# Optimization experiments

Hardware: AMD Instinct MI355X
Metric: run time of the kernel (lower is better)

The kernel has to match this reference:

```python
import jax, jax.numpy as jnp
import numpy as np

B, S, D, H = 4, 2048, 1024, 4
HD = D // H


def setup_inputs() -> dict:
    key = jax.random.key(0)
    ks = jax.random.split(key, 6)
    s = 0.02  # init scale for projection weights
    return {
        "hidden_states": jax.random.normal(ks[0], (B, S, D), jnp.float32),
        "Wq": jax.random.normal(ks[1], (D, D), jnp.float32) * s,
        "Wk": jax.random.normal(ks[2], (D, D), jnp.float32) * s,
        "Wv": jax.random.normal(ks[3], (D, D), jnp.float32) * s,
        "Wo": jax.random.normal(ks[4], (D, D), jnp.float32) * s,
        "bo": jnp.zeros((D,), jnp.float32),
        "betas": jax.random.normal(ks[5], (1, H, 1, 1), jnp.float32),
        "mem": jnp.zeros((H, HD, HD), jnp.float32),
        "z": jnp.zeros((H, HD, 1), jnp.float32),
    }


def reference(hidden_states, Wq, Wk, Wv, Wo, bo, betas, mem, z):
    b, s, d = hidden_states.shape
    h = betas.shape[1]
    hd = d // h

    def split(x):  # [b,s,d] -> [b,h,s,hd]
        return x.reshape(b, s, h, hd).transpose(0, 2, 1, 3)

    q = split(hidden_states @ Wq.T)
    k = split(hidden_states @ Wk.T)
    v = split(hidden_states @ Wv.T)

    # standard causal attention (note: no 1/sqrt(d) scaling, faithful to source)
    aw = jnp.einsum('bhqd,bhkd->bhqk', q, k)
    causal = jnp.tril(jnp.ones((s, s), bool))
    aw = jnp.where(causal, aw, jnp.finfo(aw.dtype).min)
    p = jax.nn.softmax(aw, axis=-1)
    attn = jnp.einsum('bhqk,bhkd->bhqd', p, v)

    # linear-attention memory read
    sq = jax.nn.elu(q) + 1.0
    sk = jax.nn.elu(k) + 1.0
    A_mem = jnp.einsum('bhsd,hde->bhse', sq, mem) / (
        jnp.einsum('bhsd,hdo->bhso', sq, z) + 1e-6)

    # sigmoid-gated blend
    g = jax.nn.sigmoid(betas)
    out = g * A_mem + (1.0 - g) * attn

    # memory / z state update (delta rule), averaged over batch
    delta = jnp.einsum('bhsd,hde->bhse', sk, mem) / (
        jnp.einsum('bhsd,hdo->bhso', sk, z) + 1e-6)
    mem_new = mem + jnp.einsum('bhsd,bhse->hde', sk, v - delta) / b
    z_new = z + jnp.mean(jnp.sum(sk, axis=2), axis=0)[:, :, None]

    # merge heads + output projection
    out = out.transpose(0, 2, 1, 3).reshape(b, s, d)
    out = out @ Wo.T + bo
    return (out, mem_new, z_new)
```

## Files before the change

kernel.cpp:

```cpp
#include <hip/hip_runtime.h>

#define Bsz 4
#define Ssz 2048
#define Dsz 1024
#define Hsz 4
#define HDsz 256
#define Msz 8192
#define LOG2E 1.4426950408889634f

typedef unsigned short u16;
typedef __attribute__((ext_vector_type(8))) short bf16x8;
typedef __attribute__((ext_vector_type(4))) float f32x4;

__device__ __forceinline__ u16 f2b(float f) {
  unsigned u = __float_as_uint(f);
  return (u16)((u + 0x7FFFu + ((u >> 16) & 1u)) >> 16);
}
__device__ __forceinline__ unsigned pk2(float a, float b) {
  return (unsigned)f2b(a) | ((unsigned)f2b(b) << 16);
}
__device__ __forceinline__ float ex2(float x) {
#if __has_builtin(__builtin_amdgcn_exp2f)
  return __builtin_amdgcn_exp2f(x);
#else
  return exp2f(x);
#endif
}

typedef const unsigned int __attribute__((address_space(1)))* gcp;
typedef unsigned int __attribute__((address_space(3)))* lcp;
__device__ __forceinline__ void gld16(const u16* g, u16* l) {
  __builtin_amdgcn_global_load_lds((gcp)g, (lcp)l, 16, 0, 0);
}

__global__ __launch_bounds__(256) void cvt_bf16(const float4* __restrict__ in,
                                                u16* __restrict__ outp) {
  size_t i = (size_t)blockIdx.x * 256 + threadIdx.x;
  float4 v = in[i];
  uint2 r; r.x = pk2(v.x, v.y); r.y = pk2(v.z, v.w);
  *(uint2*)(outp + i * 4) = r;
}

__global__ __launch_bounds__(256) void gemm_lds(const u16* __restrict__ A16,
                                                const u16* __restrict__ Wb,
                                                const float* __restrict__ bias,
                                                float* __restrict__ C32,
                                                u16* __restrict__ Cbf,
                                                float cbfs) {
  __shared__ u16 sA[128 * 64];
  __shared__ u16 sB[128 * 64];
  const int tid = threadIdx.x;
  const int lane = tid & 63, quad = lane >> 4, l15 = lane & 15;
  const int w = tid >> 6;
  const int mw = (w >> 1) * 64, nw = (w & 1) * 64;
  const int bid = blockIdx.y * 8 + blockIdx.x;
  const int nb = (bid & 7) * 64 + (bid >> 3);
  const int m0 = (nb >> 3) * 128, n0 = (nb & 7) * 128;
  const int r0 = tid >> 3;
  const int seg = ((tid & 7) ^ (r0 & 7)) * 8;
  const u16* ga0 = A16 + (size_t)(m0 + r0) * Dsz + seg;
  const u16* gb0 = Wb + (size_t)(n0 + r0) * Dsz + seg;
  f32x4 acc[4][4] = {};
  for (int k0 = 0; k0 < Dsz; k0 += 64) {
    __syncthreads();
#pragma unroll
    for (int i = 0; i < 4; ++i) {
      gld16(ga0 + (size_t)(i * 32) * Dsz + k0, sA + i * 2048 + w * 512);
      gld16(gb0 + (size_t)(i * 32) * Dsz + k0, sB + i * 2048 + w * 512);
    }
    __syncthreads();
#pragma unroll
    for (int dd = 0; dd < 2; ++dd) {
      bf16x8 af[4], bfr[4];
#pragma unroll
      for (int i = 0; i < 4; ++i) {
        const int sl = ((quad + 4 * dd) ^ (l15 & 7)) * 8;
        af[i] = *(const bf16x8*)&sA[(mw + i * 16 + l15) * 64 + sl];
        bfr[i] = *(const bf16x8*)&sB[(nw + i * 16 + l15) * 64 + sl];
      }
#pragma unroll
      for (int i = 0; i < 4; ++i)
#pragma unroll
        for (int j = 0; j < 4; ++j)
          acc[i][j] = __builtin_amdgcn_mfma_f32_16x16x32_bf16(af[i], bfr[j], acc[i][j], 0, 0, 0);
    }
  }
#pragma unroll
  for (int j = 0; j < 4; ++j) {
    const int n = n0 + nw + j * 16 + l15;
    const float bv = bias ? bias[n] : 0.f;
#pragma unroll
    for (int i = 0; i < 4; ++i) {
#pragma unroll
      for (int r = 0; r < 4; ++r) {
        const int m = m0 + mw + i * 16 + quad * 4 + r;
        const float val = acc[i][j][r] + bv;
        const size_t idx = (size_t)m * Dsz + n;
        if (C32) C32[idx] = val;
        if (Cbf) Cbf[idx] = f2b(val * cbfs);
      }
    }
  }
}

__global__ __launch_bounds__(256) void transpose_v(const float* __restrict__ V,
                                                   u16* __restrict__ Vt) {
  __shared__ u16 tile[32 * 36];
  const int t = threadIdx.x;
  const int s0 = blockIdx.x * 32, e0 = blockIdx.y * 32, bh = blockIdx.z;
  const int b = bh >> 2, h = bh & 3;
  {
    const int s_l = t >> 3, e8 = (t & 7) * 4;
    float4 v = *(const float4*)(V + ((size_t)(b * Ssz) + s0 + s_l) * Dsz + h * HDsz + e0 + e8);
    uint2 r; r.x = pk2(v.x, v.y); r.y = pk2(v.z, v.w);
    *(uint2*)&tile[s_l * 36 + e8] = r;
  }
  __syncthreads();
  {
    const int e_l = t >> 3, s4 = (t & 7) * 4;
    u16 a = tile[(s4 + 0) * 36 + e_l], b2 = tile[(s4 + 1) * 36 + e_l];
    u16 c = tile[(s4 + 2) * 36 + e_l], d = tile[(s4 + 3) * 36 + e_l];
    uint2 r; r.x = (unsigned)a | ((unsigned)b2 << 16);
    r.y = (unsigned)c | ((unsigned)d << 16);
    *(uint2*)(Vt + ((size_t)bh * HDsz + e0 + e_l) * Ssz + s0 + s4) = r;
  }
}

__global__ __launch_bounds__(256) void transpose_b16(const u16* __restrict__ src,
                                                     u16* __restrict__ dst) {
  __shared__ u16 tile[32 * 36];
  const int t = threadIdx.x;
  const int s0 = blockIdx.x * 32, c0 = blockIdx.y * 32, bh = blockIdx.z;
  const int b = bh >> 2, h = bh & 3;
  {
    const int s_l = t >> 3, c8 = (t & 7) * 4;
    uint2 v = *(const uint2*)(src + ((size_t)(b * Ssz) + s0 + s_l) * Dsz + h * HDsz + c0 + c8);
    *(uint2*)&tile[s_l * 36 + c8] = v;
  }
  __syncthreads();
  {
    const int c_l = t >> 3, s4 = (t & 7) * 4;
    u16 a = tile[(s4 + 0) * 36 + c_l], b2 = tile[(s4 + 1) * 36 + c_l];
    u16 c = tile[(s4 + 2) * 36 + c_l], d = tile[(s4 + 3) * 36 + c_l];
    uint2 r; r.x = (unsigned)a | ((unsigned)b2 << 16);
    r.y = (unsigned)c | ((unsigned)d << 16);
    *(uint2*)(dst + ((size_t)bh * HDsz + c0 + c_l) * Ssz + s0 + s4) = r;
  }
}

__global__ __launch_bounds__(256) void transpose_mem(const float* __restrict__ mem,
                                                     u16* __restrict__ memT) {
  __shared__ u16 tile[32 * 36];
  const int t = threadIdx.x;
  const int d0 = blockIdx.x * 32, e0 = blockIdx.y * 32, h = blockIdx.z;
  {
    const int d_l = t >> 3, e8 = (t & 7) * 4;
    float4 v = *(const float4*)(mem + (size_t)h * 65536 + (size_t)(d0 + d_l) * HDsz + e0 + e8);
    uint2 r; r.x = pk2(v.x, v.y); r.y = pk2(v.z, v.w);
    *(uint2*)&tile[d_l * 36 + e8] = r;
  }
  __syncthreads();
  {
    const int e_l = t >> 3, d4 = (t & 7) * 4;
    u16 a = tile[(d4 + 0) * 36 + e_l], b2 = tile[(d4 + 1) * 36 + e_l];
    u16 c = tile[(d4 + 2) * 36 + e_l], d = tile[(d4 + 3) * 36 + e_l];
    uint2 r; r.x = (unsigned)a | ((unsigned)b2 << 16);
    r.y = (unsigned)c | ((unsigned)d << 16);
    *(uint2*)(memT + (size_t)h * 65536 + (size_t)(e0 + e_l) * HDsz + d0 + d4) = r;
  }
}

__global__ __launch_bounds__(256) void attn_mfma(const u16* __restrict__ Qg,
                                                 const u16* __restrict__ Kg,
                                                 const u16* __restrict__ Vtg,
                                                 float* __restrict__ At,
                                                 float* __restrict__ Pb,
                                                 float* __restrict__ mlb) {
  static const unsigned char tab[52] = {
      (unsigned char)(31|0x80), (unsigned char)(31|0xC0),
      (unsigned char)(30|0x80), (unsigned char)(30|0xC0),
      (unsigned char)(29|0x80), (unsigned char)(29|0xC0),
      (unsigned char)(28|0x80), (unsigned char)(28|0xC0),
      (unsigned char)(27|0x80), (unsigned char)(27|0xC0),
      (unsigned char)(26|0x80), (unsigned char)(26|0xC0),
      (unsigned char)(25|0x80), (unsigned char)(25|0xC0),
      (unsigned char)(24|0x80), (unsigned char)(24|0xC0),
      (unsigned char)(23|0x80), (unsigned char)(23|0xC0),
      11,
      (unsigned char)(22|0x80), (unsigned char)(22|0xC0),
      (unsigned char)(21|0x80), (unsigned char)(21|0xC0),
      10,
      (unsigned char)(20|0x80), (unsigned char)(20|0xC0),
      (unsigned char)(19|0x80), (unsigned char)(19|0xC0),
      9,
      (unsigned char)(18|0x80), (unsigned char)(18|0xC0),
      (unsigned char)(17|0x80), (unsigned char)(17|0xC0),
      8,
      (unsigned char)(16|0x80), (unsigned char)(16|0xC0),
      (unsigned char)(15|0x80), (unsigned char)(15|0xC0),
      7,
      (unsigned char)(14|0x80), (unsigned char)(14|0xC0),
      (unsigned char)(13|0x80), (unsigned char)(13|0xC0),
      6,
      (unsigned char)(12|0x80), (unsigned char)(12|0xC0),
      5, 4, 3, 2, 1, 0};
  const int e = tab[blockIdx.x];
  const int qt = e & 63, cc = (e >> 6) & 1;
  const bool split = (e >> 7) != 0;
  const int bh = blockIdx.y, b = bh >> 2, h = bh & 3;
  const int tid = threadIdx.x, w = tid >> 6, lane = tid & 63;
  const int quad = lane >> 4, l15 = lane & 15;
  __shared__ u16 sK[2][32 * 256];
  __shared__ u16 sV[256 * 32];
  const int q0w = qt * 64 + w * 16;
  bf16x8 qf[8];
  {
    const u16* qp = Qg + ((size_t)(b * Ssz) + q0w + l15) * Dsz + h * HDsz + quad * 8;
#pragma unroll
    for (int dd = 0; dd < 8; ++dd) qf[dd] = *(const bf16x8*)(qp + dd * 32);
  }
  f32x4 o[16] = {};
  float m_old = -1e30f, l = 0.f;
  const int nkt = 2 * qt + 2, half = qt + 1;
  const int kt_lo = (split && cc) ? half : 0;
  const int kt_hi = (split && !cc) ? half : nkt;
  const u16* kstage = Kg + ((size_t)(b * Ssz) + (tid >> 5)) * Dsz + h * HDsz
                      + (((tid & 31) ^ ((tid >> 5) & 7)) << 3);
  const u16* vstage = Vtg + ((size_t)bh * HDsz + (tid >> 2)) * Ssz
                      + (((tid & 3) ^ ((tid >> 3) & 3)) << 3);
  int bufc = 0;
  {
    const u16* kp = kstage + (size_t)(kt_lo * 32) * Dsz;
#pragma unroll
    for (int i = 0; i < 4; ++i)
      gld16(kp + (size_t)i * 8 * Dsz, &sK[0][w * 512 + i * 2048]);
  }
  for (int kt = kt_lo; kt < kt_hi; ++kt) {
    const int j0 = kt * 32;
    __syncthreads();
    {
      const u16* vp = vstage + kt * 32;
#pragma unroll
      for (int i = 0; i < 4; ++i)
        gld16(vp + (size_t)i * 64 * Ssz, &sV[w * 512 + i * 2048]);
    }
    if (kt + 1 < kt_hi) {
      const u16* kp = kstage + (size_t)((kt + 1) * 32) * Dsz;
      const int bn = bufc ^ 1;
#pragma unroll
      for (int i = 0; i < 4; ++i)
        gld16(kp + (size_t)i * 8 * Dsz, &sK[bn][w * 512 + i * 2048]);
    }
    f32x4 s0a = {}, s0b = {}, s1a = {}, s1b = {};
#pragma unroll
    for (int dd = 0; dd < 4; ++dd) {
      const int c0 = ((dd * 4 + quad) ^ (l15 & 7)) << 3;
      const int c1 = (((dd + 4) * 4 + quad) ^ (l15 & 7)) << 3;
      bf16x8 a0 = *(const bf16x8*)&sK[bufc][l15 * 256 + c0];
      bf16x8 a1 = *(const bf16x8*)&sK[bufc][(16 + l15) * 256 + c0];
      bf16x8 b0 = *(const bf16x8*)&sK[bufc][l15 * 256 + c1];
      bf16x8 b1 = *(const bf16x8*)&sK[bufc][(16 + l15) * 256 + c1];
      s0a = __builtin_amdgcn_mfma_f32_16x16x32_bf16(a0, qf[dd], s0a, 0, 0, 0);
      s1a = __builtin_amdgcn_mfma_f32_16x16x32_bf16(a1, qf[dd], s1a, 0, 0, 0);
      s0b = __builtin_amdgcn_mfma_f32_16x16x32_bf16(b0, qf[dd + 4], s0b, 0, 0, 0);
      s1b = __builtin_amdgcn_mfma_f32_16x16x32_bf16(b1, qf[dd + 4], s1b, 0, 0, 0);
    }
    f32x4 s0v = s0a + s0b, s1v = s1a + s1b;
    const int qg = q0w + l15;
    float p[8];
#pragma unroll
    for (int r = 0; r < 4; ++r) {
      const int kg = j0 + quad * 4 + r;
      p[r] = (kg <= qg) ? s0v[r] : -1e30f;
      p[4 + r] = (kg + 16 <= qg) ? s1v[r] : -1e30f;
    }
    float mt = fmaxf(fmaxf(fmaxf(p[0], p[1]), fmaxf(p[2], p[3])),
                     fmaxf(fmaxf(p[4], p[5]), fmaxf(p[6], p[7])));
    mt = fmaxf(mt, __shfl_xor(mt, 16));
    mt = fmaxf(mt, __shfl_xor(mt, 32));
    const bool keep = __all(mt - m_old <= 11.0f);
    const float m_new = keep ? m_old : fmaxf(m_old, mt);
    float ts = 0.f;
#pragma unroll
    for (int i = 0; i < 8; ++i) { p[i] = ex2(p[i] - m_new); ts += p[i]; }
    ts += __shfl_xor(ts, 16);
    ts += __shfl_xor(ts, 32);
    if (keep) {
      l += ts;
    } else {
      const float alpha = ex2(m_old - m_new);
      l = l * alpha + ts;
      m_old = m_new;
      const float a0_ = __shfl(alpha, (lane & 48) | (quad * 4 + 0));
      const float a1_ = __shfl(alpha, (lane & 48) | (quad * 4 + 1));
      const float a2_ = __shfl(alpha, (lane & 48) | (quad * 4 + 2));
      const float a3_ = __shfl(alpha, (lane & 48) | (quad * 4 + 3));
#pragma unroll
      for (int ds = 0; ds < 16; ++ds) {
        o[ds][0] *= a0_; o[ds][1] *= a1_; o[ds][2] *= a2_; o[ds][3] *= a3_;
      }
    }
    const unsigned a0p = pk2(p[0], p[1]), a1p = pk2(p[2], p[3]);
    const unsigned b0p = pk2(p[4], p[5]), b1p = pk2(p[6], p[7]);
    const int sAl = l15 | ((quad & 1) << 5);
    const int sBl = sAl | 16;
    const unsigned xa0 = __shfl(a0p, sAl), xa1 = __shfl(a1p, sAl);
    const unsigned xb0 = __shfl(b0p, sAl), xb1 = __shfl(b1p, sAl);
    const unsigned ya0 = __shfl(a0p, sBl), ya1 = __shfl(a1p, sBl);
    const unsigned yb0 = __shfl(b0p, sBl), yb1 = __shfl(b1p, sBl);
    const bool hi2 = quad >= 2;
    uint4 pkv;
    pkv.x = hi2 ? xb0 : xa0;
    pkv.y = hi2 ? xb1 : xa1;
    pkv.z = hi2 ? yb0 : ya0;
    pkv.w = hi2 ? yb1 : ya1;
    bf16x8 pf = *(bf16x8*)&pkv;
    const int vc0 = (quad ^ ((l15 >> 1) & 3)) << 3;
    __syncthreads();
#pragma unroll
    for (int ds = 0; ds < 16; ++ds) {
      bf16x8 bv = *(const bf16x8*)&sV[(ds * 16 + l15) * 32 + vc0];
      o[ds] = __builtin_amdgcn_mfma_f32_16x16x32_bf16(pf, bv, o[ds], 0, 0, 0);
    }
    bufc ^= 1;
  }
  if (!split) {
    float lr[4];
#pragma unroll
    for (int r = 0; r < 4; ++r) lr[r] = 1.f / __shfl(l, (lane & 48) | (quad * 4 + r));
    float* ob = At + ((size_t)bh * Ssz + q0w + quad * 4) * HDsz + l15;
#pragma unroll
    for (int r = 0; r < 4; ++r)
#pragma unroll
      for (int ds = 0; ds < 16; ++ds)
        ob[(size_t)r * HDsz + ds * 16] = o[ds][r] * lr[r];
  } else {
    float* dst;
    if (cc == 0)
      dst = At + ((size_t)bh * Ssz + q0w + quad * 4) * HDsz + l15;
    else
      dst = Pb + ((size_t)((bh * 20 + (qt - 12)) * 64) + w * 16 + quad * 4) * HDsz + l15;
#pragma unroll
    for (int r = 0; r < 4; ++r)
#pragma unroll
      for (int ds = 0; ds < 16; ++ds)
        dst[(size_t)r * HDsz + ds * 16] = o[ds][r];
    if (lane < 16) {
      const int idx = (bh * 20 + (qt - 12)) * 64 + w * 16 + l15;
      mlb[cc * 40960 + idx] = m_old;
      mlb[cc * 40960 + 20480 + idx] = l;
    }
  }
}

__global__ __launch_bounds__(256) void attn_merge(float* __restrict__ At,
                                                  const float* __restrict__ Pb,
                                                  const float* __restrict__ mlb) {
  const int qx = blockIdx.x, bh = blockIdx.y;
  const int t = threadIdx.x;
  const int slot = (bh * 20 + qx) * 64;
  float4* abase = (float4*)(At + ((size_t)bh * Ssz + (12 + qx) * 64) * HDsz);
  const float4* pbase = (const float4*)(Pb + (size_t)slot * HDsz);
#pragma unroll
  for (int i = 0; i < 16; ++i) {
    const int f = i * 256 + t;
    const int qr = f >> 6;
    const int idx = slot + qr;
    const float m0 = mlb[idx], l0 = mlb[20480 + idx];
    const float m1 = mlb[40960 + idx], l1 = mlb[61440 + idx];
    const float mm = fmaxf(m0, m1);
    const float w0 = ex2(m0 - mm), w1 = ex2(m1 - mm);
    const float inv = 1.f / (l0 * w0 + l1 * w1);
    float4 av = abase[f];
    float4 pv = pbase[f];
    float4 ov;
    ov.x = (av.x * w0 + pv.x * w1) * inv;
    ov.y = (av.y * w0 + pv.y * w1) * inv;
    ov.z = (av.z * w0 + pv.z * w1) * inv;
    ov.w = (av.w * w0 + pv.w * w1) * inv;
    abase[f] = ov;
  }
}

__global__ __launch_bounds__(256) void eludens(float* __restrict__ Qb,
                                               float* __restrict__ Kb,
                                               const float* __restrict__ z,
                                               float* __restrict__ dq,
                                               float* __restrict__ dk,
                                               u16* __restrict__ SQb,
                                               u16* __restrict__ SKb) {
  const int wid = threadIdx.x >> 6, lane = threadIdx.x & 63;
  const int r = blockIdx.x * 4 + wid;
  const int b = r >> 13, h = (r >> 11) & 3, s = r & 2047;
  const size_t base = ((size_t)(b * Ssz + s)) * Dsz + h * HDsz + lane * 4;
  float4 z4 = *(const float4*)(z + h * HDsz + lane * 4);
  float4 q = *(float4*)(Qb + base);
  q.x = q.x > 0.f ? q.x + 1.f : __expf(q.x);
  q.y = q.y > 0.f ? q.y + 1.f : __expf(q.y);
  q.z = q.z > 0.f ? q.z + 1.f : __expf(q.z);
  q.w = q.w > 0.f ? q.w + 1.f : __expf(q.w);
  *(float4*)(Qb + base) = q;
  { uint2 qb; qb.x = pk2(q.x, q.y); qb.y = pk2(q.z, q.w);
    *(uint2*)(SQb + base) = qb; }
  float4 k = *(float4*)(Kb + base);
  k.x = k.x > 0.f ? k.x + 1.f : __expf(k.x);
  k.y = k.y > 0.f ? k.y + 1.f : __expf(k.y);
  k.z = k.z > 0.f ? k.z + 1.f : __expf(k.z);
  k.w = k.w > 0.f ? k.w + 1.f : __expf(k.w);
  *(float4*)(Kb + base) = k;
  { uint2 kb; kb.x = pk2(k.x, k.y); kb.y = pk2(k.z, k.w);
    *(uint2*)(SKb + base) = kb; }
  float pq = q.x * z4.x + q.y * z4.y + q.z * z4.z + q.w * z4.w;
  float pk = k.x * z4.x + k.y * z4.y + k.z * z4.z + k.w * z4.w;
#pragma unroll
  for (int off = 32; off; off >>= 1) {
    pq += __shfl_down(pq, off);
    pk += __shfl_down(pk, off);
  }
  if (lane == 0) { dq[r] = pq; dk[r] = pk; }
}

__global__ __launch_bounds__(256) void memread_mfma(const u16* __restrict__ A16,
                                                    const u16* __restrict__ memT,
                                                    const float* __restrict__ dens,
                                                    const float* __restrict__ betas,
                                                    const float* __restrict__ At,
                                                    const float* __restrict__ Vb,
                                                    u16* __restrict__ bfout, int mode) {
  __shared__ u16 sA[128 * 64];
  __shared__ u16 sB[128 * 64];
  const int h = blockIdx.z;
  const int tid = threadIdx.x, lane = tid & 63, w = tid >> 6;
  const int quad = lane >> 4, l15 = lane & 15;
  const int mw = (w >> 1) * 64, ew = (w & 1) * 64;
  const int m0 = blockIdx.y * 128, e0t = blockIdx.x * 128;
  const int r0 = tid >> 3;
  const int seg = ((tid & 7) ^ (r0 & 7)) * 8;
  const u16* ga0 = A16 + (size_t)(m0 + r0) * Dsz + h * HDsz + seg;
  const u16* gb0 = memT + (size_t)h * 65536 + (size_t)(e0t + r0) * HDsz + seg;
  f32x4 acc[4][4] = {};
  for (int k0 = 0; k0 < HDsz; k0 += 64) {
    __syncthreads();
#pragma unroll
    for (int i = 0; i < 4; ++i) {
      gld16(ga0 + (size_t)(i * 32) * Dsz + k0, sA + i * 2048 + w * 512);
      gld16(gb0 + (size_t)(i * 32) * HDsz + k0, sB + i * 2048 + w * 512);
    }
    __syncthreads();
#pragma unroll
    for (int dd = 0; dd < 2; ++dd) {
      bf16x8 af[4], bfr[4];
#pragma unroll
      for (int i = 0; i < 4; ++i) {
        const int sl = ((quad + 4 * dd) ^ (l15 & 7)) * 8;
        af[i] = *(const bf16x8*)&sA[(mw + i * 16 + l15) * 64 + sl];
        bfr[i] = *(const bf16x8*)&sB[(ew + i * 16 + l15) * 64 + sl];
      }
#pragma unroll
      for (int i = 0; i < 4; ++i)
#pragma unroll
        for (int j = 0; j < 4; ++j)
          acc[i][j] = __builtin_amdgcn_mfma_f32_16x16x32_bf16(af[i], bfr[j], acc[i][j], 0, 0, 0);
    }
  }
  const float g = 1.f / (1.f + __expf(-betas[h]));
#pragma unroll
  for (int i = 0; i < 4; ++i) {
#pragma unroll
    for (int r = 0; r < 4; ++r) {
      const int m = m0 + mw + i * 16 + quad * 4 + r;
      const int b = m >> 11, s = m & 2047;
      const int rowidx = ((b << 2) + h) * Ssz + s;
      const float inv = 1.f / (dens[rowidx] + 1e-6f);
#pragma unroll
      for (int j = 0; j < 4; ++j) {
        const int e = e0t + ew + j * 16 + l15;
        const float av = acc[i][j][r] * inv;
        if (mode == 0) {
          const float a = At[(size_t)rowidx * HDsz + e];
          bfout[(size_t)m * Dsz + h * HDsz + e] = f2b(g * av + (1.f - g) * a);
        } else {
          const float vv = Vb[(size_t)m * Dsz + h * HDsz + e];
          bfout[(size_t)m * Dsz + h * HDsz + e] = f2b(vv - av);
        }
      }
    }
  }
}

__global__ __launch_bounds__(256) void mem_update_mfma(const u16* __restrict__ SKt,
                                                       const u16* __restrict__ Wt,
                                                       float* __restrict__ P) {
  __shared__ u16 sA[128 * 64];
  __shared__ u16 sB[128 * 64];
  const int de = blockIdx.x;
  const int d0 = (de >> 1) * 128, e0 = (de & 1) * 128;
  const int h = blockIdx.y, chunk = blockIdx.z;
  const int b = chunk >> 2, s0 = (chunk & 3) * 512;
  const int bh = b * 4 + h;
  const int tid = threadIdx.x, lane = tid & 63, w = tid >> 6;
  const int quad = lane >> 4, l15 = lane & 15;
  const int dw = (w >> 1) * 64, ew = (w & 1) * 64;
  const int r0 = tid >> 3;
  const int seg = ((tid & 7) ^ (r0 & 7)) * 8;
  const u16* ga0 = SKt + ((size_t)bh * HDsz + d0 + r0) * Ssz + s0 + seg;
  const u16* gb0 = Wt + ((size_t)bh * HDsz + e0 + r0) * Ssz + s0 + seg;
  f32x4 acc[4][4] = {};
  for (int kk = 0; kk < 512; kk += 64) {
    __syncthreads();
#pragma unroll
    for (int i = 0; i < 4; ++i) {
      gld16(ga0 + (size_t)(i * 32) * Ssz + kk, sA + i * 2048 + w * 512);
      gld16(gb0 + (size_t)(i * 32) * Ssz + kk, sB + i * 2048 + w * 512);
    }
    __syncthreads();
#pragma unroll
    for (int dd = 0; dd < 2; ++dd) {
      bf16x8 af[4], bfr[4];
#pragma unroll
      for (int i = 0; i < 4; ++i) {
        const int sl = ((quad + 4 * dd) ^ (l15 & 7)) * 8;
        af[i] = *(const bf16x8*)&sA[(dw + i * 16 + l15) * 64 + sl];
        bfr[i] = *(const bf16x8*)&sB[(ew + i * 16 + l15) * 64 + sl];
      }
#pragma unroll
      for (int i = 0; i < 4; ++i)
#pragma unroll
        for (int j = 0; j < 4; ++j)
          acc[i][j] = __builtin_amdgcn_mfma_f32_16x16x32_bf16(af[i], bfr[j], acc[i][j], 0, 0, 0);
    }
  }
  float* Pp = P + ((size_t)(h * 16 + chunk)) * 65536;
#pragma unroll
  for (int i = 0; i < 4; ++i)
#pragma unroll
    for (int r = 0; r < 4; ++r) {
      const int d = d0 + dw + i * 16 + quad * 4 + r;
#pragma unroll
      for (int j = 0; j < 4; ++j) {
        const int e = e0 + ew + j * 16 + l15;
        Pp[(size_t)d * HDsz + e] = acc[i][j][r];
      }
    }
}

__global__ __launch_bounds__(256) void mem_reduce(const float4* __restrict__ P,
                                                  const float4* __restrict__ mem,
                                                  float4* __restrict__ outmem) {
  const int gid = blockIdx.x * 256 + threadIdx.x;
  const int h = gid >> 14, off = gid & 16383;
  float sx = 0.f, sy = 0.f, sz = 0.f, sw = 0.f;
#pragma unroll 4
  for (int c = 0; c < 16; ++c) {
    float4 v = P[((size_t)(h * 16 + c) << 14) + off];
    sx += v.x; sy += v.y; sz += v.z; sw += v.w;
  }
  float4 m = mem[gid];
  float4 o;
  o.x = m.x + 0.25f * sx; o.y = m.y + 0.25f * sy;
  o.z = m.z + 0.25f * sz; o.w = m.w + 0.25f * sw;
  outmem[gid] = o;
}

__global__ __launch_bounds__(256) void z_update(const float* __restrict__ SK,
                                                const float* __restrict__ z_in,
                                                float* __restrict__ z_out) {
  __shared__ float4 red[256];
  const int h = blockIdx.x >> 7, chunk = blockIdx.x & 127;
  const int wid = threadIdx.x >> 6, lane = threadIdx.x & 63;
  const int m0 = chunk * 64;
  float4 s = {0.f, 0.f, 0.f, 0.f};
#pragma unroll
  for (int i = 0; i < 16; ++i) {
    const int row = m0 + i * 4 + wid;
    float4 v = *(const float4*)(SK + (size_t)row * Dsz + h * HDsz + lane * 4);
    s.x += v.x; s.y += v.y; s.z += v.z; s.w += v.w;
  }
  red[wid * 64 + lane] = s;
  __syncthreads();
  if (wid == 0) {
    float4 a = red[lane], b = red[64 + lane], c = red[128 + lane], d = red[192 + lane];
    a.x = (a.x + b.x + c.x + d.x) * 0.25f;
    a.y = (a.y + b.y + c.y + d.y) * 0.25f;
    a.z = (a.z + b.z + c.z + d.z) * 0.25f;
    a.w = (a.w + b.w + c.w + d.w) * 0.25f;
    if (chunk == 0) {
      const float4 z4 = *(const float4*)(z_in + h * HDsz + lane * 4);
      a.x += z4.x; a.y += z4.y; a.z += z4.z; a.w += z4.w;
    }
    float* zp = z_out + h * HDsz + lane * 4;
    atomicAdd(zp + 0, a.x);
    atomicAdd(zp + 1, a.y);
    atomicAdd(zp + 2, a.z);
    atomicAdd(zp + 3, a.w);
  }
}

extern "C" void kernel_launch(void* const* d_in, const int* in_sizes, int n_in,
                              void* d_out, int out_size, void* d_ws, size_t ws_size,
                              hipStream_t stream) {
  (void)in_sizes; (void)n_in; (void)out_size; (void)ws_size;
  const float* Hs = (const float*)d_in[0];
  const float* Wq = (const float*)d_in[1];
  const float* Wk = (const float*)d_in[2];
  const float* Wv = (const float*)d_in[3];
  const float* Wo = (const float*)d_in[4];
  const float* bo = (const float*)d_in[5];
  const float* betas = (const float*)d_in[6];
  const float* mem = (const float*)d_in[7];
  const float* z = (const float*)d_in[8];

  float* ws = (float*)d_ws;
  float* Qb = ws;
  float* Kb = ws + 8388608;
  float* Vb = ws + 16777216;
  float* At = ws + 25165824;
  float* dq = ws + 33554432;
  float* dk = ws + 33587200;
  float* mlb = ws + 33619968;
  u16* ub = (u16*)(ws + 33701888);
  u16* Wqb = ub;
  u16* Wkb = ub + 1048576;
  u16* Wvb = ub + 2097152;
  u16* Wob = ub + 3145728;
  u16* Qbf = ub + 4194304;
  u16* Kbf = ub + 12582912;
  u16* Vt = ub + 20971520;
  u16* Hsb = Vt;
  u16* SQb = ub + 29360128;
  u16* memT = ub + 37748736;
  u16* SKb = Kbf;
  u16* SKt = Vt;
  u16* Wb16 = (u16*)At;
  u16* Wt = (u16*)Qb;
  float* Pb = (float*)d_out;
  float* P = (float*)d_out;

  float* out = (float*)d_out;
  float* outmem = out + (size_t)Msz * Dsz;
  float* outz = outmem + Hsz * HDsz * HDsz;

  hipMemsetAsync(outz, 0, (size_t)(Hsz * HDsz) * sizeof(float), stream);

  cvt_bf16<<<1024, 256, 0, stream>>>((const float4*)Wq, Wqb);
  cvt_bf16<<<1024, 256, 0, stream>>>((const float4*)Wk, Wkb);
  cvt_bf16<<<1024, 256, 0, stream>>>((const float4*)Wv, Wvb);
  cvt_bf16<<<1024, 256, 0, stream>>>((const float4*)Wo, Wob);
  cvt_bf16<<<8192, 256, 0, stream>>>((const float4*)Hs, Hsb);
  transpose_mem<<<dim3(8, 8, 4), 256, 0, stream>>>(mem, memT);

  dim3 gg(8, 64);
  gemm_lds<<<gg, 256, 0, stream>>>(Hsb, Wqb, nullptr, Qb, Qbf, LOG2E);
  gemm_lds<<<gg, 256, 0, stream>>>(Hsb, Wkb, nullptr, Kb, Kbf, 1.f);
  gemm_lds<<<gg, 256, 0, stream>>>(Hsb, Wvb, nullptr, Vb, nullptr, 1.f);

  transpose_v<<<dim3(64, 8, 16), 256, 0, stream>>>(Vb, Vt);
  attn_mfma<<<dim3(52, 16), 256, 0, stream>>>(Qbf, Kbf, Vt, At, Pb, mlb);
  attn_merge<<<dim3(20, 16), 256, 0, stream>>>(At, Pb, mlb);

  eludens<<<8192, 256, 0, stream>>>(Qb, Kb, z, dq, dk, SQb, SKb);
  transpose_b16<<<dim3(64, 8, 16), 256, 0, stream>>>(SKb, SKt);

  memread_mfma<<<dim3(2, 64, 4), 256, 0, stream>>>(SQb, memT, dq, betas, At, nullptr, Qbf, 0);
  memread_mfma<<<dim3(2, 64, 4), 256, 0, stream>>>(SKb, memT, dk, betas, nullptr, Vb, Wb16, 1);
  transpose_b16<<<dim3(64, 8, 16), 256, 0, stream>>>(Wb16, Wt);

  mem_update_mfma<<<dim3(4, 4, 16), 256, 0, stream>>>(SKt, Wt, P);
  mem_reduce<<<256, 256, 0, stream>>>((const float4*)P, (const float4*)mem, (float4*)outmem);
  z_update<<<512, 256, 0, stream>>>(Kb, z, outz);

  gemm_lds<<<gg, 256, 0, stream>>>(Qbf, Wob, bo, out, nullptr, 1.f);
}
```

Baseline: 487.1 us.

## Fuse ELU feature map and denominators into Q/K projection GEMM epilogue

The Q and K projection GEMMs now compute elu+1 in their epilogue. They write the bf16 feature maps directly and accumulate the z-dot denominators with wave shuffles plus atomics. This removes the standalone eludens kernel and the fp32 Q/K stores and reloads. z_update now reads the bf16 SK instead of fp32, and the four weight conversions are merged into one launch. The cost is atomic adds into dq/dk, which need an extra memset, and summing z from bf16-rounded values, which loses some precision.

```diff
diff --git a/kernel.cpp b/kernel.cpp
--- a/kernel.cpp
+++ b/kernel.cpp
@@ -19,6 +19,9 @@
 __device__ __forceinline__ unsigned pk2(float a, float b) {
   return (unsigned)f2b(a) | ((unsigned)f2b(b) << 16);
 }
+__device__ __forceinline__ float b2f(unsigned lo16) {
+  return __uint_as_float(lo16 << 16);
+}
 __device__ __forceinline__ float ex2(float x) {
 #if __has_builtin(__builtin_amdgcn_exp2f)
   return __builtin_amdgcn_exp2f(x);
@@ -41,12 +44,28 @@
   *(uint2*)(outp + i * 4) = r;
 }
 
+__global__ __launch_bounds__(256) void cvt_w4(const float4* __restrict__ w0,
+                                              const float4* __restrict__ w1,
+                                              const float4* __restrict__ w2,
+                                              const float4* __restrict__ w3,
+                                              u16* __restrict__ outp) {
+  const int blk = blockIdx.x, wsel = blk >> 10;
+  const float4* src = (wsel == 0) ? w0 : (wsel == 1) ? w1 : (wsel == 2) ? w2 : w3;
+  const size_t i = (size_t)(blk & 1023) * 256 + threadIdx.x;
+  float4 v = src[i];
+  uint2 r; r.x = pk2(v.x, v.y); r.y = pk2(v.z, v.w);
+  *(uint2*)(outp + (size_t)wsel * 1048576 + i * 4) = r;
+}
+
 __global__ __launch_bounds__(256) void gemm_lds(const u16* __restrict__ A16,
                                                 const u16* __restrict__ Wb,
                                                 const float* __restrict__ bias,
                                                 float* __restrict__ C32,
                                                 u16* __restrict__ Cbf,
-                                                float cbfs) {
+                                                float cbfs,
+                                                u16* __restrict__ selu,
+                                                float* __restrict__ dens,
+                                                const float* __restrict__ zvec) {
   __shared__ u16 sA[128 * 64];
   __shared__ u16 sB[128 * 64];
   const int tid = threadIdx.x;
@@ -85,19 +104,53 @@
           acc[i][j] = __builtin_amdgcn_mfma_f32_16x16x32_bf16(af[i], bfr[j], acc[i][j], 0, 0, 0);
     }
   }
-#pragma unroll
-  for (int j = 0; j < 4; ++j) {
-    const int n = n0 + nw + j * 16 + l15;
-    const float bv = bias ? bias[n] : 0.f;
+  if (dens) {
+    const int h = n0 >> 8;
+    float zq[4];
+#pragma unroll
+    for (int j = 0; j < 4; ++j)
+      zq[j] = zvec[h * HDsz + ((n0 & 255) + nw + j * 16 + l15)];
 #pragma unroll
     for (int i = 0; i < 4; ++i) {
 #pragma unroll
       for (int r = 0; r < 4; ++r) {
         const int m = m0 + mw + i * 16 + quad * 4 + r;
-        const float val = acc[i][j][r] + bv;
-        const size_t idx = (size_t)m * Dsz + n;
-        if (C32) C32[idx] = val;
-        if (Cbf) Cbf[idx] = f2b(val * cbfs);
+        float pdv = 0.f;
+#pragma unroll
+        for (int j = 0; j < 4; ++j) {
+          const int n = n0 + nw + j * 16 + l15;
+          const float val = acc[i][j][r];
+          const float sv = val > 0.f ? val + 1.f : __expf(val);
+          const size_t idx = (size_t)m * Dsz + n;
+          Cbf[idx] = f2b(val * cbfs);
+          selu[idx] = f2b(sv);
+          pdv += sv * zq[j];
+        }
+        pdv += __shfl_xor(pdv, 1);
+        pdv += __shfl_xor(pdv, 2);
+        pdv += __shfl_xor(pdv, 4);
+        pdv += __shfl_xor(pdv, 8);
+        if (l15 == 0) {
+          const int b = m >> 11, s = m & 2047;
+          atomicAdd(dens + ((b << 2) + h) * Ssz + s, pdv);
+        }
+      }
+    }
+  } else {
+#pragma unroll
+    for (int j = 0; j < 4; ++j) {
+      const int n = n0 + nw + j * 16 + l15;
+      const float bv = bias ? bias[n] : 0.f;
+#pragma unroll
+      for (int i = 0; i < 4; ++i) {
+#pragma unroll
+        for (int r = 0; r < 4; ++r) {
+          const int m = m0 + mw + i * 16 + quad * 4 + r;
+          const float val = acc[i][j][r] + bv;
+          const size_t idx = (size_t)m * Dsz + n;
+          if (C32) C32[idx] = val;
+          if (Cbf) Cbf[idx] = f2b(val * cbfs);
+        }
       }
     }
   }
@@ -382,44 +435,6 @@
   }
 }
 
-__global__ __launch_bounds__(256) void eludens(float* __restrict__ Qb,
-                                               float* __restrict__ Kb,
-                                               const float* __restrict__ z,
-                                               float* __restrict__ dq,
-                                               float* __restrict__ dk,
-                                               u16* __restrict__ SQb,
-                                               u16* __restrict__ SKb) {
-  const int wid = threadIdx.x >> 6, lane = threadIdx.x & 63;
-  const int r = blockIdx.x * 4 + wid;
-  const int b = r >> 13, h = (r >> 11) & 3, s = r & 2047;
-  const size_t base = ((size_t)(b * Ssz + s)) * Dsz + h * HDsz + lane * 4;
-  float4 z4 = *(const float4*)(z + h * HDsz + lane * 4);
-  float4 q = *(float4*)(Qb + base);
-  q.x = q.x > 0.f ? q.x + 1.f : __expf(q.x);
-  q.y = q.y > 0.f ? q.y + 1.f : __expf(q.y);
-  q.z = q.z > 0.f ? q.z + 1.f : __expf(q.z);
-  q.w = q.w > 0.f ? q.w + 1.f : __expf(q.w);
-  *(float4*)(Qb + base) = q;
-  { uint2 qb; qb.x = pk2(q.x, q.y); qb.y = pk2(q.z, q.w);
-    *(uint2*)(SQb + base) = qb; }
-  float4 k = *(float4*)(Kb + base);
-  k.x = k.x > 0.f ? k.x + 1.f : __expf(k.x);
-  k.y = k.y > 0.f ? k.y + 1.f : __expf(k.y);
-  k.z = k.z > 0.f ? k.z + 1.f : __expf(k.z);
-  k.w = k.w > 0.f ? k.w + 1.f : __expf(k.w);
-  *(float4*)(Kb + base) = k;
-  { uint2 kb; kb.x = pk2(k.x, k.y); kb.y = pk2(k.z, k.w);
-    *(uint2*)(SKb + base) = kb; }
-  float pq = q.x * z4.x + q.y * z4.y + q.z * z4.z + q.w * z4.w;
-  float pk = k.x * z4.x + k.y * z4.y + k.z * z4.z + k.w * z4.w;
-#pragma unroll
-  for (int off = 32; off; off >>= 1) {
-    pq += __shfl_down(pq, off);
-    pk += __shfl_down(pk, off);
-  }
-  if (lane == 0) { dq[r] = pq; dk[r] = pk; }
-}
-
 __global__ __launch_bounds__(256) void memread_mfma(const u16* __restrict__ A16,
                                                     const u16* __restrict__ memT,
                                                     const float* __restrict__ dens,
@@ -562,7 +577,7 @@
   outmem[gid] = o;
 }
 
-__global__ __launch_bounds__(256) void z_update(const float* __restrict__ SK,
+__global__ __launch_bounds__(256) void z_update(const u16* __restrict__ SKb,
                                                 const float* __restrict__ z_in,
                                                 float* __restrict__ z_out) {
   __shared__ float4 red[256];
@@ -573,8 +588,11 @@
 #pragma unroll
   for (int i = 0; i < 16; ++i) {
     const int row = m0 + i * 4 + wid;
-    float4 v = *(const float4*)(SK + (size_t)row * Dsz + h * HDsz + lane * 4);
-    s.x += v.x; s.y += v.y; s.z += v.z; s.w += v.w;
+    uint2 v = *(const uint2*)(SKb + (size_t)row * Dsz + h * HDsz + lane * 4);
+    s.x += b2f(v.x & 0xFFFFu);
+    s.y += __uint_as_float(v.x & 0xFFFF0000u);
+    s.z += b2f(v.y & 0xFFFFu);
+    s.w += __uint_as_float(v.y & 0xFFFF0000u);
   }
   red[wid * 64 + lane] = s;
   __syncthreads();
@@ -629,7 +647,7 @@
   u16* Hsb = Vt;
   u16* SQb = ub + 29360128;
   u16* memT = ub + 37748736;
-  u16* SKb = Kbf;
+  u16* SKb = (u16*)Kb;
   u16* SKt = Vt;
   u16* Wb16 = (u16*)At;
   u16* Wt = (u16*)Qb;
@@ -641,24 +659,22 @@
   float* outz = outmem + Hsz * HDsz * HDsz;
 
   hipMemsetAsync(outz, 0, (size_t)(Hsz * HDsz) * sizeof(float), stream);
-
-  cvt_bf16<<<1024, 256, 0, stream>>>((const float4*)Wq, Wqb);
-  cvt_bf16<<<1024, 256, 0, stream>>>((const float4*)Wk, Wkb);
-  cvt_bf16<<<1024, 256, 0, stream>>>((const float4*)Wv, Wvb);
-  cvt_bf16<<<1024, 256, 0, stream>>>((const float4*)Wo, Wob);
+  hipMemsetAsync(dq, 0, (size_t)65536 * sizeof(float), stream);
+
+  cvt_w4<<<4096, 256, 0, stream>>>((const float4*)Wq, (const float4*)Wk,
+                                   (const float4*)Wv, (const float4*)Wo, ub);
   cvt_bf16<<<8192, 256, 0, stream>>>((const float4*)Hs, Hsb);
   transpose_mem<<<dim3(8, 8, 4), 256, 0, stream>>>(mem, memT);
 
   dim3 gg(8, 64);
-  gemm_lds<<<gg, 256, 0, stream>>>(Hsb, Wqb, nullptr, Qb, Qbf, LOG2E);
-  gemm_lds<<<gg, 256, 0, stream>>>(Hsb, Wkb, nullptr, Kb, Kbf, 1.f);
-  gemm_lds<<<gg, 256, 0, stream>>>(Hsb, Wvb, nullptr, Vb, nullptr, 1.f);
+  gemm_lds<<<gg, 256, 0, stream>>>(Hsb, Wqb, nullptr, nullptr, Qbf, LOG2E, SQb, dq, z);
+  gemm_lds<<<gg, 256, 0, stream>>>(Hsb, Wkb, nullptr, nullptr, Kbf, 1.f, SKb, dk, z);
+  gemm_lds<<<gg, 256, 0, stream>>>(Hsb, Wvb, nullptr, Vb, nullptr, 1.f, nullptr, nullptr, nullptr);
 
   transpose_v<<<dim3(64, 8, 16), 256, 0, stream>>>(Vb, Vt);
   attn_mfma<<<dim3(52, 16), 256, 0, stream>>>(Qbf, Kbf, Vt, At, Pb, mlb);
   attn_merge<<<dim3(20, 16), 256, 0, stream>>>(At, Pb, mlb);
 
-  eludens<<<8192, 256, 0, stream>>>(Qb, Kb, z, dq, dk, SQb, SKb);
   transpose_b16<<<dim3(64, 8, 16), 256, 0, stream>>>(SKb, SKt);
 
   memread_mfma<<<dim3(2, 64, 4), 256, 0, stream>>>(SQb, memT, dq, betas, At, nullptr, Qbf, 0);
@@ -667,7 +683,7 @@
 
   mem_update_mfma<<<dim3(4, 4, 16), 256, 0, stream>>>(SKt, Wt, P);
   mem_reduce<<<256, 256, 0, stream>>>((const float4*)P, (const float4*)mem, (float4*)outmem);
-  z_update<<<512, 256, 0, stream>>>(Kb, z, outz);
-
-  gemm_lds<<<gg, 256, 0, stream>>>(Qbf, Wob, bo, out, nullptr, 1.f);
-}
+  z_update<<<512, 256, 0, stream>>>(SKb, z, outz);
+
+  gemm_lds<<<gg, 256, 0, stream>>>(Qbf, Wob, bo, out, nullptr, 1.f, nullptr, nullptr, nullptr);
+}
```

After: 445.6 us. -8.5%, faster.
